# Kernel tuning notes

Hardware: AMD Instinct MI355X
Metric: run time of the kernel (lower is better)

## Reference

```python
import jax, jax.numpy as jnp
import numpy as np

NH = 6
D = 78  # dim_k = dim_v, dk = dv = 13 per head
SCALE = 1.0 / np.sqrt(D // NH).astype(np.float32)


def _split(t):
    # (B, n, D) -> (B, H, n, dk)
    B, n, d = t.shape
    return t.reshape(B, n, NH, d // NH).transpose(0, 2, 1, 3)


def _merge(t):
    # (B, H, n, dk) -> (B, n, D)
    B, h, n, d = t.shape
    return t.transpose(0, 2, 1, 3).reshape(B, n, h * d)


def _cross_attn(x, y, Wq, Wk, Wv):
    # MultiHeadCrossSelfAttention / MultiHeadSelfAttention math (dropout=identity in eval;
    # attn_mask is expanded but never applied in the original forward).
    q = _split(x @ Wq)
    k = _split(y @ Wk)
    v = _split(y @ Wv)
    dist = jax.nn.softmax(jnp.einsum('bhqd,bhkd->bhqk', q, k) * SCALE, axis=-1)
    return _merge(jnp.einsum('bhqk,bhkd->bhqd', dist, v))


def _contrastive_attn(x, y, Wq, Wk, Wv):
    # MultiHeadContrastiveSelfAttention: softmax -> (1 - p) -> softmax -> matmul, residual q add.
    q = _split(x @ Wq)
    k = _split(y @ Wk)
    v = _split(y @ Wv)
    dist = jax.nn.softmax(jnp.einsum('bhqd,bhkd->bhqk', q, k) * SCALE, axis=-1)
    dist = jax.nn.softmax(1.0 - dist, axis=-1)
    return _merge(q + jnp.einsum('bhqk,bhkd->bhqd', dist, v))


def setup_inputs() -> dict:
    key = jax.random.key(0)
    ks = jax.random.split(key, 20)
    B, nT, nV, nA = 8, 1024, 1024, 1024
    inp = {
        'x': jax.random.normal(ks[0], (B, nT, D), jnp.float32),
        'y': jax.random.normal(ks[1], (B, nV, D), jnp.float32),
        'z': jax.random.normal(ks[2], (B, nA, D), jnp.float32),
        'mask_tv': jnp.zeros((B, nT, nV), jnp.bool_),
        'mask_ta': jnp.zeros((B, nT, nA), jnp.bool_),
    }
    names = ['Wq_tv', 'Wk_tv', 'Wv_tv', 'Wq_ta', 'Wk_ta', 'Wv_ta',
             'Wq_ctv', 'Wk_ctv', 'Wv_ctv', 'Wq_cta', 'Wk_cta', 'Wv_cta',
             'Wq_s', 'Wk_s', 'Wv_s']
    for i, nm in enumerate(names):
        inp[nm] = jax.random.normal(ks[3 + i], (D, D), jnp.float32) * 0.05
    return inp


def reference(x, y, z, mask_tv, mask_ta,
              Wq_tv, Wk_tv, Wv_tv, Wq_ta, Wk_ta, Wv_ta,
              Wq_ctv, Wk_ctv, Wv_ctv, Wq_cta, Wk_cta, Wv_cta,
              Wq_s, Wk_s, Wv_s):
    # masks are dead args in the original module (expanded but never applied)
    att_tv = _cross_attn(x, y, Wq_tv, Wk_tv, Wv_tv)          # MHSCA_TV
    att_ta = _cross_attn(x, z, Wq_ta, Wk_ta, Wv_ta)          # MHSCA_TA
    c_tv = _contrastive_attn(x, y, Wq_ctv, Wk_ctv, Wv_ctv)   # MHSCTA_TV
    c_ta = _contrastive_attn(x, z, Wq_cta, Wk_cta, Wv_cta)   # MHSCTA_TA
    # fuse three pooled modality tokens through the length-3 MHSA
    tokens = jnp.stack([x.mean(axis=1),
                        (att_tv + c_tv).mean(axis=1),
                        (att_ta + c_ta).mean(axis=1)], axis=1)  # (B, 3, D)
    fused = _cross_attn(tokens, tokens, Wq_s, Wk_s, Wv_s)       # MHSA
    # (B, 4*1024 + 3, D)
    return jnp.concatenate([att_tv, c_tv, att_ta, c_ta, fused], axis=1)
```

## Files before the change

### kernel.cpp

```cpp
#include <hip/hip_runtime.h>
#include <hip/hip_bf16.h>

#define BB 8
#define NN 1024
#define DM 78
#define NH 6
#define DK 13
#define NROW 4099
#define QSCL 0.40013158f
#define SCALE 0.27735009811261457f
#define INV1023 0.000977517106549365f

using bf16 = __hip_bfloat16;
typedef __attribute__((ext_vector_type(8))) short short8;
typedef __attribute__((ext_vector_type(4))) short short4v;
typedef __attribute__((ext_vector_type(4))) float f32x4;

#if __has_builtin(__builtin_amdgcn_exp2f)
#define EXP2(x) __builtin_amdgcn_exp2f(x)
#else
__device__ __forceinline__ float EXP2(float x) {
    float r;
    asm volatile("v_exp_f32 %0, %1\n\ts_nop 1" : "=v"(r) : "v"(x));
    return r;
}
#endif

#define SMFMA(k, q, c) __builtin_amdgcn_mfma_f32_16x16x16bf16_1k((k), (q), (c), 0, 0, 0)

#define MATSZ ((size_t)48 * 1024 * 16)

struct PW { const float* w[12]; };

__device__ __forceinline__ unsigned pkbf2(float a, float b) {
    __hip_bfloat162 t = __float22bfloat162_rn(make_float2(a, b));
    return *(unsigned*)&t;
}

union FRAG { unsigned u[4]; short8 s8; };

__global__ __launch_bounds__(256, 6) void proj_kernel(const float* __restrict__ x,
                                                      const float* __restrict__ y,
                                                      const float* __restrict__ z,
                                                      PW p,
                                                      unsigned* __restrict__ Qbf,
                                                      unsigned* __restrict__ Kbf,
                                                      unsigned* __restrict__ Vt,
                                                      float* __restrict__ Qf32,
                                                      float* __restrict__ sv,
                                                      float* __restrict__ tok) {
    __shared__ unsigned SMEM[6608];
    int bid = blockIdx.x;
    int tid = threadIdx.x;
    int mat = bid >> 7;
    int rb = bid & 127;
    const float* src = (mat < 4) ? x : (((mat - 4) & 1) ? z : y);
    const float* sp = src + (size_t)rb * 64 * DM;
    const float* W = p.w[mat];
    int bb = rb >> 4;
    int i0 = (rb & 15) * 64;
    float* CT = (float*)SMEM;

    unsigned* ALu = SMEM;
    unsigned* WTu = SMEM + 64 * 52;
    const float2* sp2 = (const float2*)sp;
    for (int i = tid; i < 64 * 39; i += 256) {
        float2 f2 = sp2[i];
        int r = i / 39, pc = i - r * 39;
        ALu[r * 52 + pc] = pkbf2(f2.x, f2.y);
    }
    for (int i = tid; i < 64 * 13; i += 256) {
        int r = i / 13, pc = i - r * 13;
        ALu[r * 52 + 39 + pc] = 0u;
    }
    for (int i = tid; i < 41 * 80; i += 256) {
        int pc = i / 80, n = i - pc * 80;
        int k0 = pc * 2;
        float a = (n < DM && k0 < DM) ? W[(size_t)k0 * DM + n] : 0.f;
        float bv = (n < DM && k0 + 1 < DM) ? W[(size_t)(k0 + 1) * DM + n] : 0.f;
        WTu[n * 41 + pc] = pkbf2(a, bv);
    }
    __syncthreads();
    if (mat == 0 && tid < 39) {
        const unsigned* col = ALu + tid;
        float s0 = 0.f, s1 = 0.f;
        for (int r = 0; r < 64; ++r) {
            unsigned u = col[r * 52];
            s0 += __uint_as_float(u << 16);
            s1 += __uint_as_float(u & 0xffff0000u);
        }
        atomicAdd(&tok[bb * DM + tid * 2], s0);
        atomicAdd(&tok[bb * DM + tid * 2 + 1], s1);
    }
    int wv = tid >> 6, lane = tid & 63, quad = lane >> 4, lq = lane & 15;
    int r0 = wv * 16;
    const short* ALs = (const short*)ALu;
    const short* WTs = (const short*)WTu;
    short8 af0 = *(const short8*)(ALs + (r0 + lq) * 104 + quad * 8);
    short8 af1 = *(const short8*)(ALs + (r0 + lq) * 104 + 32 + quad * 8);
    short8 af2 = *(const short8*)(ALs + (r0 + lq) * 104 + 64 + quad * 8);
    const f32x4 zz = {0.f, 0.f, 0.f, 0.f};
    f32x4 acc[5];
#pragma unroll
    for (int n = 0; n < 5; ++n) acc[n] = zz;
#pragma unroll
    for (int n = 0; n < 5; ++n) {
        const short* wb = WTs + (n * 16 + lq) * 82 + quad * 8;
        acc[n] = __builtin_amdgcn_mfma_f32_16x16x32_bf16(
            af0, *(const short8*)wb, acc[n], 0, 0, 0);
        acc[n] = __builtin_amdgcn_mfma_f32_16x16x32_bf16(
            af1, *(const short8*)(wb + 32), acc[n], 0, 0, 0);
        acc[n] = __builtin_amdgcn_mfma_f32_16x16x32_bf16(
            af2, *(const short8*)(wb + 64), acc[n], 0, 0, 0);
    }
    __syncthreads();
#pragma unroll
    for (int n = 0; n < 5; ++n) {
        int c = n * 16 + lq;
        if (c < DM) {
#pragma unroll
            for (int r = 0; r < 4; ++r)
                CT[(r0 + quad * 4 + r) * 81 + c] = acc[n][r];
        }
    }
    __syncthreads();
    if (mat < 8) {
        unsigned* dst = (mat < 4) ? Qbf : Kbf;
        int m4 = (mat < 4) ? mat : mat - 4;
        float scl = (mat < 4) ? QSCL : 1.0f;
        for (int t2 = tid; t2 < NH * 64 * 8; t2 += 256) {
            int hh = t2 >> 9;
            int rem = t2 & 511;
            int r = rem >> 3, cp = rem & 7;
            int c0 = cp * 2, c1 = cp * 2 + 1;
            float a = (c0 < DK) ? CT[r * 81 + hh * DK + c0] * scl : 0.f;
            float bv = (c1 < DK) ? CT[r * 81 + hh * DK + c1] * scl : 0.f;
            dst[(((size_t)m4 * 48 + bb * NH + hh) * 1024 + i0 + r) * 8 + cp] = pkbf2(a, bv);
        }
        if (mat >= 2 && mat < 4) {
            for (int t2 = tid; t2 < 64 * DM; t2 += 256) {
                int r = t2 / DM, c = t2 - r * DM;
                int hh = c / DK, dd = c - hh * DK;
                Qf32[((size_t)(mat - 2) * 48 + bb * NH + hh) * 1024 * DK +
                     (size_t)(i0 + r) * DK + dd] = CT[r * 81 + c];
            }
        }
    } else {
        for (int t2 = tid; t2 < NH * 16 * 32; t2 += 256) {
            int hh = t2 >> 9;
            int rem = t2 & 511;
            int dd = rem >> 5, cp = rem & 31;
            int pp = (cp & 15) * 2;
            int b2 = cp >> 4;
            int qd = pp >> 3, jj = pp & 7;
            int l0 = b2 * 32 + 4 * qd + (jj < 4 ? jj : 12 + jj);
            float a, bv;
            if (dd < DK) {
                a = CT[l0 * 81 + hh * DK + dd];
                bv = CT[(l0 + 1) * 81 + hh * DK + dd];
            } else if (dd == 13) { a = 1.f; bv = 1.f; }
            else { a = 0.f; bv = 0.f; }
            Vt[(((size_t)(mat - 8) * 48 + bb * NH + hh) * 16 + dd) * 512 +
               (i0 >> 1) + cp] = pkbf2(a, bv);
        }
        if (mat >= 10 && tid < DM) {
            int hh = tid / DK, dd = tid - hh * DK;
            float s = 0.f;
            for (int r = 0; r < 64; ++r) s += CT[r * 81 + tid];
            atomicAdd(&sv[((size_t)(mat - 10) * 48 + bb * NH + hh) * DK + dd], s);
        }
    }
}

__global__ __launch_bounds__(256) void att_kernel(const bf16* __restrict__ Qbf,
                                                  const bf16* __restrict__ Kbf,
                                                  const bf16* __restrict__ Vt,
                                                  const float* __restrict__ Qf32,
                                                  const float* __restrict__ sv,
                                                  float* __restrict__ tok,
                                                  float* __restrict__ out) {
    int bid = blockIdx.x;
    int qt = (bid >> 3) & 7;
    int ghb = (bid & 7) | ((bid >> 6) << 3);
    int h = ghb % NH;
    int r2 = ghb / NH;
    int b = r2 & 7;
    int g = r2 >> 3;
    int tid = threadIdx.x, wave = tid >> 6, lane = tid & 63;
    int quad = lane >> 4, lq = lane & 15;
    size_t mb = (size_t)g * 48 + b * NH + h;
    int q0 = qt * 64 + wave * 16;
    int q1 = q0 + 512;

    const short* Kp = (const short*)Kbf + mb * 1024 * 16;
    const short* Vp = (const short*)Vt + mb * 16 * 1024 + (size_t)lq * 1024;
    f32x4 OA = {0.f, 0.f, 0.f, 0.f};
    f32x4 OB = {0.f, 0.f, 0.f, 0.f};
    const f32x4 zz = {0.f, 0.f, 0.f, 0.f};

    short4v qfA = *(const short4v*)((const short*)Qbf + (mb * 1024 + q0 + lq) * 16 + quad * 4);
    short4v qfB = *(const short4v*)((const short*)Qbf + (mb * 1024 + q1 + lq) * 16 + quad * 4);
    int ko = quad * 4;

    short4v kX0a = *(const short4v*)(Kp + lq * 16 + ko);
    short4v kX1a = *(const short4v*)(Kp + 256 + lq * 16 + ko);
    short4v kY0a = *(const short4v*)(Kp + 512 + lq * 16 + ko);
    short4v kY1a = *(const short4v*)(Kp + 768 + lq * 16 + ko);
    short8 vXa = *(const short8*)(Vp + quad * 8);
    short8 vYa = *(const short8*)(Vp + 32 + quad * 8);
    short4v kX0b = *(const short4v*)(Kp + 1024 + lq * 16 + ko);
    short4v kX1b = *(const short4v*)(Kp + 1280 + lq * 16 + ko);
    short4v kY0b = *(const short4v*)(Kp + 1536 + lq * 16 + ko);
    short4v kY1b = *(const short4v*)(Kp + 1792 + lq * 16 + ko);
    short8 vXb = *(const short8*)(Vp + 64 + quad * 8);
    short8 vYb = *(const short8*)(Vp + 96 + quad * 8);

    const short* Kit = Kp + 2048;
    const short* Vit = Vp + 128;

#pragma unroll
    for (int kt = 0; kt < 16; ++kt) {
        __builtin_amdgcn_s_setprio(1);
        f32x4 SX0 = SMFMA(kX0a, qfA, zz);
        f32x4 SX1 = SMFMA(kX1a, qfA, zz);
        f32x4 SX2 = SMFMA(kX0a, qfB, zz);
        f32x4 SX3 = SMFMA(kX1a, qfB, zz);
        f32x4 SY0 = SMFMA(kY0a, qfA, zz);
        f32x4 SY1 = SMFMA(kY1a, qfA, zz);
        f32x4 SY2 = SMFMA(kY0a, qfB, zz);
        f32x4 SY3 = SMFMA(kY1a, qfB, zz);
        __builtin_amdgcn_s_setprio(0);
        short4v kX0n = *(const short4v*)(Kit + lq * 16 + ko);
        short4v kX1n = *(const short4v*)(Kit + 256 + lq * 16 + ko);
        short4v kY0n = *(const short4v*)(Kit + 512 + lq * 16 + ko);
        short4v kY1n = *(const short4v*)(Kit + 768 + lq * 16 + ko);
        short8 vXn = *(const short8*)(Vit + quad * 8);
        short8 vYn = *(const short8*)(Vit + 32 + quad * 8);
        Kit += 1024; Vit += 64;

        FRAG aXA, aXB, aYA, aYB;
        aXA.u[0] = pkbf2(EXP2(SX0[0]), EXP2(SX0[1]));
        aXA.u[1] = pkbf2(EXP2(SX0[2]), EXP2(SX0[3]));
        aXA.u[2] = pkbf2(EXP2(SX1[0]), EXP2(SX1[1]));
        aXA.u[3] = pkbf2(EXP2(SX1[2]), EXP2(SX1[3]));
        OA = __builtin_amdgcn_mfma_f32_16x16x32_bf16(aXA.s8, vXa, OA, 0, 0, 0);
        aXB.u[0] = pkbf2(EXP2(SX2[0]), EXP2(SX2[1]));
        aXB.u[1] = pkbf2(EXP2(SX2[2]), EXP2(SX2[3]));
        aXB.u[2] = pkbf2(EXP2(SX3[0]), EXP2(SX3[1]));
        aXB.u[3] = pkbf2(EXP2(SX3[2]), EXP2(SX3[3]));
        OB = __builtin_amdgcn_mfma_f32_16x16x32_bf16(aXB.s8, vXa, OB, 0, 0, 0);
        aYA.u[0] = pkbf2(EXP2(SY0[0]), EXP2(SY0[1]));
        aYA.u[1] = pkbf2(EXP2(SY0[2]), EXP2(SY0[3]));
        aYA.u[2] = pkbf2(EXP2(SY1[0]), EXP2(SY1[1]));
        aYA.u[3] = pkbf2(EXP2(SY1[2]), EXP2(SY1[3]));
        OA = __builtin_amdgcn_mfma_f32_16x16x32_bf16(aYA.s8, vYa, OA, 0, 0, 0);
        aYB.u[0] = pkbf2(EXP2(SY2[0]), EXP2(SY2[1]));
        aYB.u[1] = pkbf2(EXP2(SY2[2]), EXP2(SY2[3]));
        aYB.u[2] = pkbf2(EXP2(SY3[0]), EXP2(SY3[1]));
        aYB.u[3] = pkbf2(EXP2(SY3[2]), EXP2(SY3[3]));
        OB = __builtin_amdgcn_mfma_f32_16x16x32_bf16(aYB.s8, vYa, OB, 0, 0, 0);
        kX0a = kX0b; kX1a = kX1b; kY0a = kY0b; kY1a = kY1b; vXa = vXb; vYa = vYb;
        kX0b = kX0n; kX1b = kX1n; kY0b = kY0n; kY1b = kY1n; vXb = vXn; vYb = vYn;
    }

    size_t rowbase = (g == 0) ? 0 : (g == 1 ? 2 * NN : (g == 2 ? NN : 3 * NN));
    float lA[4], lB[4];
#pragma unroll
    for (int r = 0; r < 4; ++r) {
        lA[r] = __shfl(OA[r], (lane & 48) | 13, 64);
        lB[r] = __shfl(OB[r], (lane & 48) | 13, 64);
    }
    float svv = 0.f;
    const float* qf32p = nullptr;
    if (g >= 2) {
        if (lq < DK) svv = sv[((size_t)(g - 2) * 48 + b * NH + h) * DK + lq];
        qf32p = Qf32 + ((size_t)(g - 2) * 48 + b * NH + h) * 1024 * DK + lq;
    }
    float vsum = 0.f;
#pragma unroll
    for (int r = 0; r < 4; ++r) {
        int mA = q0 + quad * 4 + r;
        int mB = q1 + quad * 4 + r;
        float A0 = OA[r] / lA[r];
        float A1 = OB[r] / lB[r];
        float v0, v1;
        if (g < 2) { v0 = A0; v1 = A1; }
        else {
            float qr0 = (lq < DK) ? qf32p[(size_t)mA * DK] : 0.f;
            float qr1 = (lq < DK) ? qf32p[(size_t)mB * DK] : 0.f;
            v0 = qr0 + (svv - A0) * INV1023;
            v1 = qr1 + (svv - A1) * INV1023;
        }
        if (lq < DK) {
            out[((size_t)b * NROW + rowbase + mA) * DM + h * DK + lq] = v0;
            out[((size_t)b * NROW + rowbase + mB) * DM + h * DK + lq] = v1;
            vsum += v0 + v1;
        }
    }
    vsum += __shfl_xor(vsum, 16);
    vsum += __shfl_xor(vsum, 32);
    if (quad == 0 && lq < DK) {
        int tki = (g & 1) ? 2 : 1;
        atomicAdd(&tok[(size_t)tki * (8 * DM) + b * DM + h * DK + lq], vsum);
    }
}

__global__ __launch_bounds__(256) void fused_kernel(const float* __restrict__ tok,
                                                    const float* __restrict__ Wq,
                                                    const float* __restrict__ Wk,
                                                    const float* __restrict__ Wv,
                                                    float* __restrict__ out) {
    __shared__ float T[3 * DM], Qs[3 * DM], Ks[3 * DM], Vs[3 * DM], P[NH * 9];
    int b = blockIdx.x, tid = threadIdx.x;
    if (tid < 234) {
        int t = tid / DM, d = tid - t * DM;
        T[tid] = tok[(size_t)t * (8 * DM) + b * DM + d] * (1.f / NN);
    }
    __syncthreads();
    for (int idx = tid; idx < 702; idx += 256) {
        int mat = idx / 234;
        int rem = idx - mat * 234;
        int t = rem / DM, d = rem - t * DM;
        const float* W = (mat == 0) ? Wq : (mat == 1 ? Wk : Wv);
        float a = 0.f;
        for (int e = 0; e < DM; ++e) a = fmaf(T[t * DM + e], W[(size_t)e * DM + d], a);
        float* dst = (mat == 0) ? Qs : (mat == 1 ? Ks : Vs);
        dst[t * DM + d] = a;
    }
    __syncthreads();
    if (tid < NH * 3) {
        int h = tid / 3, t = tid % 3;
        float s[3];
        for (int k = 0; k < 3; ++k) {
            float a = 0.f;
            for (int d2 = 0; d2 < DK; ++d2)
                a += Qs[t * DM + h * DK + d2] * Ks[k * DM + h * DK + d2];
            s[k] = a * SCALE;
        }
        float mm = fmaxf(s[0], fmaxf(s[1], s[2]));
        float e0 = __expf(s[0] - mm), e1 = __expf(s[1] - mm), e2 = __expf(s[2] - mm);
        float inv = 1.f / (e0 + e1 + e2);
        P[(h * 3 + t) * 3 + 0] = e0 * inv;
        P[(h * 3 + t) * 3 + 1] = e1 * inv;
        P[(h * 3 + t) * 3 + 2] = e2 * inv;
    }
    __syncthreads();
    if (tid < 234) {
        int t = tid / DM, d = tid - t * DM, h = d / DK;
        float a = 0.f;
        for (int k = 0; k < 3; ++k) a += P[(h * 3 + t) * 3 + k] * Vs[k * DM + d];
        out[((size_t)b * NROW + 4 * NN + t) * DM + d] = a;
    }
}

extern "C" void kernel_launch(void* const* d_in, const int* in_sizes, int n_in,
                              void* d_out, int out_size, void* d_ws, size_t ws_size,
                              hipStream_t stream) {
    const float* bigs[3] = {nullptr, nullptr, nullptr};
    const float* w[15];
    int nb = 0, nw = 0;
    for (int i = 0; i < n_in; ++i) {
        if (in_sizes[i] == BB * NN * DM && nb < 3) bigs[nb++] = (const float*)d_in[i];
        else if (in_sizes[i] == DM * DM && nw < 15) w[nw++] = (const float*)d_in[i];
    }
    if (nb < 3 || nw < 15) {
        bigs[0] = (const float*)d_in[0]; bigs[1] = (const float*)d_in[1];
        bigs[2] = (const float*)d_in[2];
        int base = (n_in >= 20) ? 5 : 3;
        for (int i = 0; i < 15; ++i) w[i] = (const float*)d_in[base + i];
    }
    const float* x = bigs[0];
    const float* y = bigs[1];
    const float* z = bigs[2];
    float* out = (float*)d_out;

    bf16* Qbf = (bf16*)d_ws;
    bf16* Kbf = Qbf + 4 * MATSZ;
    bf16* Vt  = Kbf + 4 * MATSZ;
    float* Qf32 = (float*)(Vt + 4 * MATSZ);
    float* sv = Qf32 + (size_t)2 * 48 * 1024 * DK;
    float* tok = sv + 2 * 48 * DK;

    PW pp;
    const float* wsel[12] = {w[0], w[3], w[6], w[9],
                             w[1], w[4], w[7], w[10],
                             w[2], w[5], w[8], w[11]};
    for (int i = 0; i < 12; ++i) pp.w[i] = wsel[i];

    hipMemsetAsync(sv, 0, (2 * 48 * DK + 3 * 8 * DM) * sizeof(float), stream);
    proj_kernel<<<1536, 256, 0, stream>>>(x, y, z, pp, (unsigned*)Qbf, (unsigned*)Kbf,
                                          (unsigned*)Vt, Qf32, sv, tok);
    att_kernel<<<4 * BB * NH * 8, 256, 0, stream>>>(Qbf, Kbf, Vt, Qf32, sv, tok, out);
    fused_kernel<<<BB, 256, 0, stream>>>(tok, w[12], w[13], w[14], out);
}
```

Measured before the change: 208.9 us.

## Single-stage K/V prefetch in attention loop and parallelize column reductions

The attention inner loop drops from two-deep to one-deep register prefetch of K and V fragments and is no longer force-unrolled, which cuts register pressure and code size. The column-sum reductions in the projection kernel (token means and V sums) are split across several thread segments, each issuing its own atomicAdd, to shorten the serial loop. The trade-off is less memory-latency hiding in the attention loop and more atomics in exchange for better occupancy and a shorter reduction tail.

```diff
diff --git a/kernel.cpp b/kernel.cpp
--- a/kernel.cpp
+++ b/kernel.cpp
@@ -81,16 +81,19 @@
         WTu[n * 41 + pc] = pkbf2(a, bv);
     }
     __syncthreads();
-    if (mat == 0 && tid < 39) {
-        const unsigned* col = ALu + tid;
+    if (mat == 0 && tid < 156) {
+        int pc = tid % 39, seg = tid / 39;
+        const unsigned* col = ALu + pc;
         float s0 = 0.f, s1 = 0.f;
-        for (int r = 0; r < 64; ++r) {
-            unsigned u = col[r * 52];
+        int rA = seg * 16;
+#pragma unroll
+        for (int r = 0; r < 16; ++r) {
+            unsigned u = col[(rA + r) * 52];
             s0 += __uint_as_float(u << 16);
             s1 += __uint_as_float(u & 0xffff0000u);
         }
-        atomicAdd(&tok[bb * DM + tid * 2], s0);
-        atomicAdd(&tok[bb * DM + tid * 2 + 1], s1);
+        atomicAdd(&tok[bb * DM + pc * 2], s0);
+        atomicAdd(&tok[bb * DM + pc * 2 + 1], s1);
     }
     int wv = tid >> 6, lane = tid & 63, quad = lane >> 4, lq = lane & 15;
     int r0 = wv * 16;
@@ -163,10 +166,12 @@
             Vt[(((size_t)(mat - 8) * 48 + bb * NH + hh) * 16 + dd) * 512 +
                (i0 >> 1) + cp] = pkbf2(a, bv);
         }
-        if (mat >= 10 && tid < DM) {
-            int hh = tid / DK, dd = tid - hh * DK;
+        if (mat >= 10 && tid < 234) {
+            int c = tid % 78, seg = tid / 78;
+            int rA = seg * 22, rB = (seg == 2) ? 64 : rA + 22;
             float s = 0.f;
-            for (int r = 0; r < 64; ++r) s += CT[r * 81 + tid];
+            for (int r = rA; r < rB; ++r) s += CT[r * 81 + c];
+            int hh = c / DK, dd = c - hh * DK;
             atomicAdd(&sv[((size_t)(mat - 10) * 48 + bb * NH + hh) * DK + dd], s);
         }
     }
@@ -201,66 +206,57 @@
     short4v qfA = *(const short4v*)((const short*)Qbf + (mb * 1024 + q0 + lq) * 16 + quad * 4);
     short4v qfB = *(const short4v*)((const short*)Qbf + (mb * 1024 + q1 + lq) * 16 + quad * 4);
     int ko = quad * 4;
-
-    short4v kX0a = *(const short4v*)(Kp + lq * 16 + ko);
-    short4v kX1a = *(const short4v*)(Kp + 256 + lq * 16 + ko);
-    short4v kY0a = *(const short4v*)(Kp + 512 + lq * 16 + ko);
-    short4v kY1a = *(const short4v*)(Kp + 768 + lq * 16 + ko);
-    short8 vXa = *(const short8*)(Vp + quad * 8);
-    short8 vYa = *(const short8*)(Vp + 32 + quad * 8);
-    short4v kX0b = *(const short4v*)(Kp + 1024 + lq * 16 + ko);
-    short4v kX1b = *(const short4v*)(Kp + 1280 + lq * 16 + ko);
-    short4v kY0b = *(const short4v*)(Kp + 1536 + lq * 16 + ko);
-    short4v kY1b = *(const short4v*)(Kp + 1792 + lq * 16 + ko);
-    short8 vXb = *(const short8*)(Vp + 64 + quad * 8);
-    short8 vYb = *(const short8*)(Vp + 96 + quad * 8);
-
-    const short* Kit = Kp + 2048;
-    const short* Vit = Vp + 128;
-
-#pragma unroll
+    short4v kX0 = *(const short4v*)(Kp + lq * 16 + ko);
+    short4v kX1 = *(const short4v*)(Kp + (16 + lq) * 16 + ko);
+    short4v kY0 = *(const short4v*)(Kp + (32 + lq) * 16 + ko);
+    short4v kY1 = *(const short4v*)(Kp + (48 + lq) * 16 + ko);
+    short8 vX = *(const short8*)(Vp + quad * 8);
+    short8 vY = *(const short8*)(Vp + 32 + quad * 8);
+
+    const short* Kit = Kp + 64 * 16;
+    const short* Vit = Vp + 64;
+
     for (int kt = 0; kt < 16; ++kt) {
         __builtin_amdgcn_s_setprio(1);
-        f32x4 SX0 = SMFMA(kX0a, qfA, zz);
-        f32x4 SX1 = SMFMA(kX1a, qfA, zz);
-        f32x4 SX2 = SMFMA(kX0a, qfB, zz);
-        f32x4 SX3 = SMFMA(kX1a, qfB, zz);
-        f32x4 SY0 = SMFMA(kY0a, qfA, zz);
-        f32x4 SY1 = SMFMA(kY1a, qfA, zz);
-        f32x4 SY2 = SMFMA(kY0a, qfB, zz);
-        f32x4 SY3 = SMFMA(kY1a, qfB, zz);
+        f32x4 SX0 = SMFMA(kX0, qfA, zz);
+        f32x4 SX1 = SMFMA(kX1, qfA, zz);
+        f32x4 SX2 = SMFMA(kX0, qfB, zz);
+        f32x4 SX3 = SMFMA(kX1, qfB, zz);
+        f32x4 SY0 = SMFMA(kY0, qfA, zz);
+        f32x4 SY1 = SMFMA(kY1, qfA, zz);
+        f32x4 SY2 = SMFMA(kY0, qfB, zz);
+        f32x4 SY3 = SMFMA(kY1, qfB, zz);
         __builtin_amdgcn_s_setprio(0);
         short4v kX0n = *(const short4v*)(Kit + lq * 16 + ko);
-        short4v kX1n = *(const short4v*)(Kit + 256 + lq * 16 + ko);
-        short4v kY0n = *(const short4v*)(Kit + 512 + lq * 16 + ko);
-        short4v kY1n = *(const short4v*)(Kit + 768 + lq * 16 + ko);
+        short4v kX1n = *(const short4v*)(Kit + (16 + lq) * 16 + ko);
+        short4v kY0n = *(const short4v*)(Kit + (32 + lq) * 16 + ko);
+        short4v kY1n = *(const short4v*)(Kit + (48 + lq) * 16 + ko);
         short8 vXn = *(const short8*)(Vit + quad * 8);
         short8 vYn = *(const short8*)(Vit + 32 + quad * 8);
-        Kit += 1024; Vit += 64;
 
         FRAG aXA, aXB, aYA, aYB;
         aXA.u[0] = pkbf2(EXP2(SX0[0]), EXP2(SX0[1]));
         aXA.u[1] = pkbf2(EXP2(SX0[2]), EXP2(SX0[3]));
         aXA.u[2] = pkbf2(EXP2(SX1[0]), EXP2(SX1[1]));
         aXA.u[3] = pkbf2(EXP2(SX1[2]), EXP2(SX1[3]));
-        OA = __builtin_amdgcn_mfma_f32_16x16x32_bf16(aXA.s8, vXa, OA, 0, 0, 0);
+        OA = __builtin_amdgcn_mfma_f32_16x16x32_bf16(aXA.s8, vX, OA, 0, 0, 0);
         aXB.u[0] = pkbf2(EXP2(SX2[0]), EXP2(SX2[1]));
         aXB.u[1] = pkbf2(EXP2(SX2[2]), EXP2(SX2[3]));
         aXB.u[2] = pkbf2(EXP2(SX3[0]), EXP2(SX3[1]));
         aXB.u[3] = pkbf2(EXP2(SX3[2]), EXP2(SX3[3]));
-        OB = __builtin_amdgcn_mfma_f32_16x16x32_bf16(aXB.s8, vXa, OB, 0, 0, 0);
+        OB = __builtin_amdgcn_mfma_f32_16x16x32_bf16(aXB.s8, vX, OB, 0, 0, 0);
         aYA.u[0] = pkbf2(EXP2(SY0[0]), EXP2(SY0[1]));
         aYA.u[1] = pkbf2(EXP2(SY0[2]), EXP2(SY0[3]));
         aYA.u[2] = pkbf2(EXP2(SY1[0]), EXP2(SY1[1]));
         aYA.u[3] = pkbf2(EXP2(SY1[2]), EXP2(SY1[3]));
-        OA = __builtin_amdgcn_mfma_f32_16x16x32_bf16(aYA.s8, vYa, OA, 0, 0, 0);
+        OA = __builtin_amdgcn_mfma_f32_16x16x32_bf16(aYA.s8, vY, OA, 0, 0, 0);
         aYB.u[0] = pkbf2(EXP2(SY2[0]), EXP2(SY2[1]));
         aYB.u[1] = pkbf2(EXP2(SY2[2]), EXP2(SY2[3]));
         aYB.u[2] = pkbf2(EXP2(SY3[0]), EXP2(SY3[1]));
         aYB.u[3] = pkbf2(EXP2(SY3[2]), EXP2(SY3[3]));
-        OB = __builtin_amdgcn_mfma_f32_16x16x32_bf16(aYB.s8, vYa, OB, 0, 0, 0);
-        kX0a = kX0b; kX1a = kX1b; kY0a = kY0b; kY1a = kY1b; vXa = vXb; vYa = vYb;
-        kX0b = kX0n; kX1b = kX1n; kY0b = kY0n; kY1b = kY1n; vXb = vXn; vYb = vYn;
+        OB = __builtin_amdgcn_mfma_f32_16x16x32_bf16(aYB.s8, vY, OB, 0, 0, 0);
+        kX0 = kX0n; kX1 = kX1n; kY0 = kY0n; kY1 = kY1n; vX = vXn; vY = vYn;
+        Kit += 64 * 16; Vit += 64;
     }
 
     size_t rowbase = (g == 0) ? 0 : (g == 1 ? 2 * NN : (g == 2 ? NN : 3 * NN));
```

Result: no change. 211.8 us (+1.4%).
